# Performance work log

Hardware: AMD Instinct MI355X
Metric: run time of the kernel (lower is better)

The kernel has to match this reference:

```python
import jax, jax.numpy as jnp
import numpy as np

N, E, ND, ED, H, L = 50000, 800000, 6, 4, 128, 4


def _ln(x, g, b, eps=1e-5):
    m = x.mean(-1, keepdims=True)
    v = ((x - m) ** 2).mean(-1, keepdims=True)
    return (x - m) * jax.lax.rsqrt(v + eps) * g + b


def _block(x, w1, b1, g1, be1, w2, b2, g2, be2):
    # Linear -> LayerNorm -> GELU -> (Dropout=identity in eval) -> Linear -> LayerNorm -> GELU
    h = jax.nn.gelu(_ln(x @ w1 + b1, g1, be1), approximate=False)
    return jax.nn.gelu(_ln(h @ w2 + b2, g2, be2), approximate=False)


def setup_inputs() -> dict:
    key = jax.random.key(0)
    ks = iter(jax.random.split(key, 16))
    w = lambda *s: jax.random.normal(next(ks), s, jnp.float32) * 0.05
    z = lambda *s: jnp.zeros(s, jnp.float32)
    o = lambda *s: jnp.ones(s, jnp.float32)
    return {
        "x": jax.random.normal(next(ks), (N, ND), jnp.float32),
        "edge_index": jax.random.randint(next(ks), (2, E), 0, N),
        "edge_attr": jax.random.normal(next(ks), (E, ED), jnp.float32),
        "ne_w1": w(ND, H), "ne_b1": z(H), "ne_g1": o(H), "ne_be1": z(H),
        "ne_w2": w(H, H), "ne_b2": z(H), "ne_g2": o(H), "ne_be2": z(H),
        "ee_w1": w(ED, H), "ee_b1": z(H), "ee_g1": o(H), "ee_be1": z(H),
        "ee_w2": w(H, H), "ee_b2": z(H), "ee_g2": o(H), "ee_be2": z(H),
        "cv_w1": w(L, H, H), "cv_b1": z(L, H), "cv_g1": o(L, H), "cv_be1": z(L, H),
        "cv_w2": w(L, H, H), "cv_b2": z(L, H), "cv_g2": o(L, H), "cv_be2": z(L, H),
        "nm_g": o(L, H), "nm_b": z(L, H),
        "dh_w1": w(H, H // 2), "dh_b1": z(H // 2), "dh_g": o(H // 2), "dh_be": z(H // 2),
        "dh_w2": w(H // 2, 3), "dh_b2": z(3),
        "sh_w1": w(H, H // 2), "sh_b1": z(H // 2), "sh_g": o(H // 2), "sh_be": z(H // 2),
        "sh_w2": w(H // 2, 1), "sh_b2": z(1),
    }


def reference(x, edge_index, edge_attr,
              ne_w1, ne_b1, ne_g1, ne_be1, ne_w2, ne_b2, ne_g2, ne_be2,
              ee_w1, ee_b1, ee_g1, ee_be1, ee_w2, ee_b2, ee_g2, ee_be2,
              cv_w1, cv_b1, cv_g1, cv_be1, cv_w2, cv_b2, cv_g2, cv_be2,
              nm_g, nm_b,
              dh_w1, dh_b1, dh_g, dh_be, dh_w2, dh_b2,
              sh_w1, sh_b1, sh_g, sh_be, sh_w2, sh_b2):
    h = _block(x, ne_w1, ne_b1, ne_g1, ne_be1, ne_w2, ne_b2, ne_g2, ne_be2)           # [N, H]
    e = _block(edge_attr, ee_w1, ee_b1, ee_g1, ee_be1, ee_w2, ee_b2, ee_g2, ee_be2)   # [E, H]
    src, dst = edge_index[0], edge_index[1]
    for l in range(L):
        # GINEConv (eps=0): sum_j relu(x_j + e_ij), then MLP((1+eps)*x + aggr)
        msg = jax.nn.relu(h[src] + e)                         # [E, H] gather + edge add
        agg = jax.ops.segment_sum(msg, dst, num_segments=N)   # [N, H] scatter-add
        u = _block(h + agg, cv_w1[l], cv_b1[l], cv_g1[l], cv_be1[l],
                   cv_w2[l], cv_b2[l], cv_g2[l], cv_be2[l])
        h = h + jax.nn.gelu(_ln(u, nm_g[l], nm_b[l]), approximate=False)  # residual
    d = jax.nn.gelu(_ln(h @ dh_w1 + dh_b1, dh_g, dh_be), approximate=False)
    displacement = d @ dh_w2 + dh_b2                          # [N, 3]
    s = jax.nn.gelu(_ln(h @ sh_w1 + sh_b1, sh_g, sh_be), approximate=False)
    stress = jax.nn.softplus(s @ sh_w2 + sh_b2)               # [N, 1]
    return displacement, stress, h
```

## Files before the change

### kernel.cpp

```cpp
#include <hip/hip_runtime.h>
#include <hip/hip_bf16.h>

#define HD 128
#define TILE 64
#define ST 136

typedef __attribute__((ext_vector_type(8))) short bf16x8;
typedef __attribute__((ext_vector_type(4))) float f32x4;

__device__ __forceinline__ float gelu_f(float x) {
    float y = fabsf(x) * 0.70710678118654752f;
    float t = __builtin_amdgcn_rcpf(fmaf(0.3275911f, y, 1.0f));
    float p = t * fmaf(t, fmaf(t, fmaf(t, fmaf(t, 1.061405429f, -1.453152027f),
                                       1.421413741f), -0.284496736f), 0.254829592f);
    float E = fmaf(-p, __expf(-y * y), 1.0f);
    return 0.5f * x * (1.0f + copysignf(E, x));
}
__device__ __forceinline__ unsigned short f2bf(float f) {
    unsigned int x = __float_as_uint(f);
    x = x + 0x7fffu + ((x >> 16) & 1u);
    return (unsigned short)(x >> 16);
}
__device__ __forceinline__ unsigned int pk2bf(float lo, float hi) {
    return (unsigned int)f2bf(lo) | ((unsigned int)f2bf(hi) << 16);
}
__device__ __forceinline__ float bf2f(unsigned short u) {
    return __uint_as_float((unsigned int)u << 16);
}

__device__ __forceinline__ void mm_mfma(const unsigned short* sA, int wrow, int lane,
                                        const unsigned short* __restrict__ wt, f32x4 acc[8]) {
    int m = lane & 15, kb = lane >> 4;
    bf16x8 a[4];
#pragma unroll
    for (int kk = 0; kk < 4; ++kk)
        a[kk] = *(const bf16x8*)(sA + (wrow + m) * ST + kk * 32 + kb * 8);
#pragma unroll
    for (int n0 = 0; n0 < 8; ++n0) {
        f32x4 c = {0.f, 0.f, 0.f, 0.f};
#pragma unroll
        for (int kk = 0; kk < 4; ++kk) {
            bf16x8 b = *(const bf16x8*)(wt + ((size_t)((n0 * 4 + kk) * 64 + lane)) * 8);
            c = __builtin_amdgcn_mfma_f32_16x16x32_bf16(b, a[kk], c, 0, 0, 0);
        }
        acc[n0] = c;
    }
}

__device__ __forceinline__ void mm_mfma2(const unsigned short* sH, const unsigned short* sL,
                                         int wrow, int lane,
                                         const unsigned short* __restrict__ wt, f32x4 acc[8]) {
    int m = lane & 15, kb = lane >> 4;
    bf16x8 ah[4], al[4];
#pragma unroll
    for (int kk = 0; kk < 4; ++kk) {
        ah[kk] = *(const bf16x8*)(sH + (wrow + m) * ST + kk * 32 + kb * 8);
        al[kk] = *(const bf16x8*)(sL + (wrow + m) * ST + kk * 32 + kb * 8);
    }
#pragma unroll
    for (int n0 = 0; n0 < 8; ++n0) {
        f32x4 c = {0.f, 0.f, 0.f, 0.f};
#pragma unroll
        for (int kk = 0; kk < 4; ++kk) {
            bf16x8 b = *(const bf16x8*)(wt + ((size_t)((n0 * 4 + kk) * 64 + lane)) * 8);
            c = __builtin_amdgcn_mfma_f32_16x16x32_bf16(b, ah[kk], c, 0, 0, 0);
            c = __builtin_amdgcn_mfma_f32_16x16x32_bf16(b, al[kk], c, 0, 0, 0);
        }
        acc[n0] = c;
    }
}

__device__ __forceinline__ void bias_ln_gelu(f32x4 acc[8], float u[8][4],
                                             const float* bias, const float* g,
                                             const float* be, int kb) {
    float s = 0.f, ss = 0.f;
#pragma unroll
    for (int n0 = 0; n0 < 8; ++n0)
#pragma unroll
        for (int q = 0; q < 4; ++q) {
            float x = acc[n0][q] + bias[n0 * 16 + kb * 4 + q];
            u[n0][q] = x;
            s += x; ss += x * x;
        }
    s += __shfl_xor(s, 16); ss += __shfl_xor(ss, 16);
    s += __shfl_xor(s, 32); ss += __shfl_xor(ss, 32);
    float mean = s * (1.f / HD);
    float inv = rsqrtf(ss * (1.f / HD) - mean * mean + 1e-5f);
#pragma unroll
    for (int n0 = 0; n0 < 8; ++n0)
#pragma unroll
        for (int q = 0; q < 4; ++q) {
            int c = n0 * 16 + kb * 4 + q;
            u[n0][q] = gelu_f((u[n0][q] - mean) * inv * g[c] + be[c]);
        }
}

__global__ void prep_weights(const float* __restrict__ ne_w2, const float* __restrict__ ee_w2,
                             const float* __restrict__ cv_w1, const float* __restrict__ cv_w2,
                             unsigned short* __restrict__ wbf) {
    int mat = blockIdx.x;
    const float* src = (mat == 0) ? ne_w2
                     : (mat == 1) ? ee_w2
                     : (mat < 6)  ? cv_w1 + (size_t)(mat - 2) * HD * HD
                                  : cv_w2 + (size_t)(mat - 6) * HD * HD;
    unsigned short* dst = wbf + (size_t)mat * HD * HD;
    for (int i = threadIdx.x; i < HD * HD; i += 256) {
        int e = i & 7, lane = (i >> 3) & 63, f = i >> 9;
        int m = lane & 15, kb = lane >> 4;
        int n0 = f >> 2, kk = f & 3;
        int k = kk * 32 + kb * 8 + e;
        int c = n0 * 16 + m;
        dst[i] = f2bf(src[(size_t)k * HD + c]);
    }
}

template <int IN_DIM, bool EDGE>
__global__ __launch_bounds__(256) void encoder_mfma(
    const float* __restrict__ in, const float* __restrict__ w1,
    const float* __restrict__ b1, const float* __restrict__ g1,
    const float* __restrict__ be1, const unsigned short* __restrict__ wt2,
    const float* __restrict__ b2, const float* __restrict__ g2,
    const float* __restrict__ be2, float* __restrict__ h_out,
    unsigned short* __restrict__ e_perm, const int* __restrict__ pos, int rows) {
    __shared__ __align__(16) unsigned short s_A[TILE * ST];
    __shared__ float s_vec[6][HD];
    __shared__ int s_pos[TILE];

    int tid = threadIdx.x;
    int row0 = blockIdx.x * TILE;
    if (tid < HD) {
        s_vec[0][tid] = b1[tid]; s_vec[1][tid] = g1[tid]; s_vec[2][tid] = be1[tid];
        s_vec[3][tid] = b2[tid]; s_vec[4][tid] = g2[tid]; s_vec[5][tid] = be2[tid];
    }
    if (EDGE && tid < TILE) {
        int gr = row0 + tid;
        s_pos[tid] = (gr < rows) ? pos[gr] : 0;
    }
    __syncthreads();

    int tr = tid >> 4, tc = tid & 15;
    int r0 = tr * 4, c0 = tc * 8;
    float w1r[IN_DIM][8];
#pragma unroll
    for (int k = 0; k < IN_DIM; ++k) {
        float4 pa = *(const float4*)(w1 + (size_t)k * HD + c0);
        float4 pb = *(const float4*)(w1 + (size_t)k * HD + c0 + 4);
        w1r[k][0] = pa.x; w1r[k][1] = pa.y; w1r[k][2] = pa.z; w1r[k][3] = pa.w;
        w1r[k][4] = pb.x; w1r[k][5] = pb.y; w1r[k][6] = pb.z; w1r[k][7] = pb.w;
    }
    float v[4][8];
#pragma unroll
    for (int i = 0; i < 4; ++i)
#pragma unroll
        for (int j = 0; j < 8; ++j) v[i][j] = s_vec[0][c0 + j];
#pragma unroll
    for (int i = 0; i < 4; ++i) {
        int gr = min(row0 + r0 + i, rows - 1);
        float xr[IN_DIM];
        if constexpr (IN_DIM == 4) {
            float4 t4 = *(const float4*)(in + (size_t)gr * 4);
            xr[0] = t4.x; xr[1] = t4.y; xr[2] = t4.z; xr[3] = t4.w;
        } else {
#pragma unroll
            for (int k = 0; k < IN_DIM; ++k) xr[k] = in[(size_t)gr * IN_DIM + k];
        }
#pragma unroll
        for (int k = 0; k < IN_DIM; ++k)
#pragma unroll
            for (int j = 0; j < 8; ++j) v[i][j] = fmaf(xr[k], w1r[k][j], v[i][j]);
    }
#pragma unroll
    for (int i = 0; i < 4; ++i) {
        float s = 0.f, ss = 0.f;
#pragma unroll
        for (int j = 0; j < 8; ++j) { s += v[i][j]; ss += v[i][j] * v[i][j]; }
#pragma unroll
        for (int msk = 1; msk < 16; msk <<= 1) { s += __shfl_xor(s, msk); ss += __shfl_xor(ss, msk); }
        float mean = s * (1.f / HD);
        float inv = rsqrtf(ss * (1.f / HD) - mean * mean + 1e-5f);
#pragma unroll
        for (int j = 0; j < 8; ++j)
            v[i][j] = gelu_f((v[i][j] - mean) * inv * s_vec[1][c0 + j] + s_vec[2][c0 + j]);
        uint4 q4;
        q4.x = pk2bf(v[i][0], v[i][1]); q4.y = pk2bf(v[i][2], v[i][3]);
        q4.z = pk2bf(v[i][4], v[i][5]); q4.w = pk2bf(v[i][6], v[i][7]);
        *(uint4*)&s_A[(r0 + i) * ST + c0] = q4;
    }
    __syncthreads();

    int wave = tid >> 6, lane = tid & 63;
    int m = lane & 15, kb = lane >> 4;
    int wrow = wave * 16;
    f32x4 acc[8];
    mm_mfma(s_A, wrow, lane, wt2, acc);
    float u[8][4];
    bias_ln_gelu(acc, u, s_vec[3], s_vec[4], s_vec[5], kb);

    if (EDGE) {
        __syncthreads();
#pragma unroll
        for (int n0 = 0; n0 < 8; ++n0) {
            uint2 p;
            p.x = pk2bf(u[n0][0], u[n0][1]);
            p.y = pk2bf(u[n0][2], u[n0][3]);
            *(uint2*)&s_A[(wrow + m) * ST + n0 * 16 + kb * 4] = p;
        }
        __syncthreads();
#pragma unroll
        for (int i = 0; i < 4; ++i) {
            int c = tid + i * 256;
            int r = c >> 4, cc = (c & 15) * 8;
            int gr = row0 + r;
            if (gr < rows) {
                uint4 q4 = *(uint4*)&s_A[r * ST + cc];
                *(uint4*)(e_perm + (size_t)s_pos[r] * HD + cc) = q4;
            }
        }
    } else {
        int grow = row0 + wrow + m;
        if (grow < rows) {
#pragma unroll
            for (int n0 = 0; n0 < 8; ++n0)
                *(float4*)(h_out + (size_t)grow * HD + n0 * 16 + kb * 4) =
                    make_float4(u[n0][0], u[n0][1], u[n0][2], u[n0][3]);
        }
    }
}

__global__ __launch_bounds__(256) void conv_mfma(
    const unsigned short* __restrict__ tin_hi, const unsigned short* __restrict__ tin_lo,
    float* __restrict__ h,
    const unsigned short* __restrict__ wt1, const float* __restrict__ b1,
    const float* __restrict__ g1, const float* __restrict__ be1,
    const unsigned short* __restrict__ wt2, const float* __restrict__ b2,
    const float* __restrict__ g2, const float* __restrict__ be2,
    const float* __restrict__ nmg, const float* __restrict__ nmb, int rows) {
    __shared__ __align__(16) unsigned short s_A[TILE * ST];
    __shared__ __align__(16) unsigned short s_L[TILE * ST];
    __shared__ float s_vec[8][HD];

    int tid = threadIdx.x;
    int row0 = blockIdx.x * TILE;
    if (tid < HD) {
        s_vec[0][tid] = b1[tid];  s_vec[1][tid] = g1[tid];  s_vec[2][tid] = be1[tid];
        s_vec[3][tid] = b2[tid];  s_vec[4][tid] = g2[tid];  s_vec[5][tid] = be2[tid];
        s_vec[6][tid] = nmg[tid]; s_vec[7][tid] = nmb[tid];
    }
#pragma unroll
    for (int i = 0; i < 4; ++i) {
        int c = tid + i * 256;
        int r = c >> 4, cc = (c & 15) * 8;
        int gr = min(row0 + r, rows - 1);
        *(uint4*)&s_A[r * ST + cc] = *(const uint4*)(tin_hi + (size_t)gr * HD + cc);
        *(uint4*)&s_L[r * ST + cc] = *(const uint4*)(tin_lo + (size_t)gr * HD + cc);
    }
    __syncthreads();

    int wave = tid >> 6, lane = tid & 63;
    int m = lane & 15, kb = lane >> 4;
    int wrow = wave * 16;
    f32x4 acc[8];
    float u[8][4];

    mm_mfma2(s_A, s_L, wrow, lane, wt1, acc);
    bias_ln_gelu(acc, u, s_vec[0], s_vec[1], s_vec[2], kb);
    __syncthreads();
#pragma unroll
    for (int n0 = 0; n0 < 8; ++n0) {
        uint2 p;
        p.x = pk2bf(u[n0][0], u[n0][1]);
        p.y = pk2bf(u[n0][2], u[n0][3]);
        *(uint2*)&s_A[(wrow + m) * ST + n0 * 16 + kb * 4] = p;
    }
    __syncthreads();

    mm_mfma(s_A, wrow, lane, wt2, acc);
    bias_ln_gelu(acc, u, s_vec[3], s_vec[4], s_vec[5], kb);
    {
        float s = 0.f, ss = 0.f;
#pragma unroll
        for (int n0 = 0; n0 < 8; ++n0)
#pragma unroll
            for (int q = 0; q < 4; ++q) { s += u[n0][q]; ss += u[n0][q] * u[n0][q]; }
        s += __shfl_xor(s, 16); ss += __shfl_xor(ss, 16);
        s += __shfl_xor(s, 32); ss += __shfl_xor(ss, 32);
        float mean = s * (1.f / HD);
        float inv = rsqrtf(ss * (1.f / HD) - mean * mean + 1e-5f);
#pragma unroll
        for (int n0 = 0; n0 < 8; ++n0)
#pragma unroll
            for (int q = 0; q < 4; ++q) {
                int c = n0 * 16 + kb * 4 + q;
                u[n0][q] = gelu_f((u[n0][q] - mean) * inv * s_vec[6][c] + s_vec[7][c]);
            }
    }
    int grow = row0 + wrow + m;
    if (grow < rows) {
#pragma unroll
        for (int n0 = 0; n0 < 8; ++n0) {
            size_t idx = (size_t)grow * HD + n0 * 16 + kb * 4;
            float4 hv = *(const float4*)(h + idx);
            hv.x += u[n0][0]; hv.y += u[n0][1]; hv.z += u[n0][2]; hv.w += u[n0][3];
            *(float4*)(h + idx) = hv;
        }
    }
}

__global__ void zero_kernel(int* p, int n) {
    int i = blockIdx.x * 256 + threadIdx.x;
    if (i < n) p[i] = 0;
}
__global__ void hist_kernel(const int* __restrict__ dst, int* __restrict__ cnt, int n) {
    for (int i = blockIdx.x * 256 + threadIdx.x; i < n; i += gridDim.x * 256)
        atomicAdd(&cnt[dst[i]], 1);
}
__global__ __launch_bounds__(1024) void scan_block_kernel(
    const int* __restrict__ cnt, int* __restrict__ incl, int* __restrict__ bsum, int n) {
    __shared__ int buf[2][1024];
    int t = threadIdx.x;
    int i = blockIdx.x * 1024 + t;
    int v = (i < n) ? cnt[i] : 0;
    buf[0][t] = v;
    __syncthreads();
    int pin = 0;
    for (int off = 1; off < 1024; off <<= 1) {
        int x = buf[pin][t];
        if (t >= off) x += buf[pin][t - off];
        buf[pin ^ 1][t] = x;
        __syncthreads();
        pin ^= 1;
    }
    if (i < n) incl[i] = buf[pin][t];
    if (t == 1023) bsum[blockIdx.x] = buf[pin][t];
}
__global__ void scan_top_kernel(int* bsum, int nb) {
    int t = threadIdx.x;
    int v = (t < nb) ? bsum[t] : 0;
    int orig = v;
#pragma unroll
    for (int off = 1; off < 64; off <<= 1) {
        int y = __shfl_up(v, off);
        if (t >= off) v += y;
    }
    if (t < nb) bsum[t] = v - orig;
}
__global__ void add_off_kernel(int* __restrict__ offs, const int* __restrict__ bsum,
                               int* __restrict__ cursor, int n) {
    int i = blockIdx.x * 256 + threadIdx.x;
    if (i == 0) { offs[0] = 0; cursor[0] = 0; }
    if (i < n) {
        int v = offs[i + 1] + bsum[i >> 10];
        offs[i + 1] = v;
        if (i + 1 < n) cursor[i + 1] = v;
    }
}
__global__ void scatter_kernel(const int* __restrict__ srcArr, const int* __restrict__ dstArr,
                               int* __restrict__ cursor, int* __restrict__ pos,
                               int* __restrict__ esrc, int n) {
    for (int i = blockIdx.x * 256 + threadIdx.x; i < n; i += gridDim.x * 256) {
        int d = dstArr[i];
        int p = atomicAdd(&cursor[d], 1);
        pos[i] = p;
        esrc[p] = srcArr[i];
    }
}

__global__ __launch_bounds__(256) void aggregate_kernel(
    const float* __restrict__ h, const unsigned short* __restrict__ e,
    const int* __restrict__ offs, const int* __restrict__ esrc,
    unsigned short* __restrict__ tin_hi, unsigned short* __restrict__ tin_lo, int nnodes) {
    int wave = threadIdx.x >> 6, lane = threadIdx.x & 63;
    int n = blockIdx.x * 4 + wave;
    if (n >= nnodes) return;
    int beg = offs[n], end = offs[n + 1];
    float ax = 0.f, ay = 0.f;
    int i = beg;
    for (; i + 4 <= end; i += 4) {
        int s0 = esrc[i], s1 = esrc[i + 1], s2 = esrc[i + 2], s3 = esrc[i + 3];
        float2 h0 = *(const float2*)(h + (size_t)s0 * HD + 2 * lane);
        float2 h1 = *(const float2*)(h + (size_t)s1 * HD + 2 * lane);
        float2 h2 = *(const float2*)(h + (size_t)s2 * HD + 2 * lane);
        float2 h3 = *(const float2*)(h + (size_t)s3 * HD + 2 * lane);
        unsigned int e0 = *(const unsigned int*)(e + (size_t)(i + 0) * HD + 2 * lane);
        unsigned int e1 = *(const unsigned int*)(e + (size_t)(i + 1) * HD + 2 * lane);
        unsigned int e2 = *(const unsigned int*)(e + (size_t)(i + 2) * HD + 2 * lane);
        unsigned int e3 = *(const unsigned int*)(e + (size_t)(i + 3) * HD + 2 * lane);
        ax += fmaxf(h0.x + __uint_as_float(e0 << 16), 0.f);
        ay += fmaxf(h0.y + __uint_as_float(e0 & 0xffff0000u), 0.f);
        ax += fmaxf(h1.x + __uint_as_float(e1 << 16), 0.f);
        ay += fmaxf(h1.y + __uint_as_float(e1 & 0xffff0000u), 0.f);
        ax += fmaxf(h2.x + __uint_as_float(e2 << 16), 0.f);
        ay += fmaxf(h2.y + __uint_as_float(e2 & 0xffff0000u), 0.f);
        ax += fmaxf(h3.x + __uint_as_float(e3 << 16), 0.f);
        ay += fmaxf(h3.y + __uint_as_float(e3 & 0xffff0000u), 0.f);
    }
    for (; i < end; ++i) {
        int src = esrc[i];
        float2 hv = *(const float2*)(h + (size_t)src * HD + 2 * lane);
        unsigned int ue = *(const unsigned int*)(e + (size_t)i * HD + 2 * lane);
        ax += fmaxf(hv.x + __uint_as_float(ue << 16), 0.f);
        ay += fmaxf(hv.y + __uint_as_float(ue & 0xffff0000u), 0.f);
    }
    float2 hn = *(const float2*)(h + (size_t)n * HD + 2 * lane);
    float tx = hn.x + ax, ty = hn.y + ay;
    unsigned short hx = f2bf(tx), hy = f2bf(ty);
    float lx = tx - bf2f(hx), ly = ty - bf2f(hy);
    *(unsigned int*)(tin_hi + (size_t)n * HD + 2 * lane) =
        (unsigned int)hx | ((unsigned int)hy << 16);
    *(unsigned int*)(tin_lo + (size_t)n * HD + 2 * lane) = pk2bf(lx, ly);
}

__global__ __launch_bounds__(256) void head_kernel(
    const float* __restrict__ h, const float* __restrict__ dw1,
    const float* __restrict__ db1, const float* __restrict__ dg,
    const float* __restrict__ dbe, const float* __restrict__ dw2,
    const float* __restrict__ db2, const float* __restrict__ sw1,
    const float* __restrict__ sb1, const float* __restrict__ sg,
    const float* __restrict__ sbe, const float* __restrict__ sw2,
    const float* __restrict__ sb2, float* __restrict__ out, int nnodes) {
    __shared__ float s_wd[HD * 64];
    __shared__ float s_ws[HD * 64];
    __shared__ float s_vd[3][64];
    __shared__ float s_vs[3][64];
    __shared__ float s_w2d[64 * 3];
    __shared__ float s_w2s[64];
    __shared__ float s_h[4][HD];
    __shared__ float s_b2[4];

    int tid = threadIdx.x;
    for (int i = tid; i < HD * 64; i += 256) { s_wd[i] = dw1[i]; s_ws[i] = sw1[i]; }
    if (tid < 64) {
        s_vd[0][tid] = db1[tid]; s_vd[1][tid] = dg[tid]; s_vd[2][tid] = dbe[tid];
        s_vs[0][tid] = sb1[tid]; s_vs[1][tid] = sg[tid]; s_vs[2][tid] = sbe[tid];
        s_w2s[tid] = sw2[tid];
    }
    if (tid < 64 * 3) s_w2d[tid] = dw2[tid];
    if (tid == 0) { s_b2[0] = db2[0]; s_b2[1] = db2[1]; s_b2[2] = db2[2]; s_b2[3] = sb2[0]; }
    __syncthreads();

    int wave = tid >> 6, lane = tid & 63;
    float* disp = out;
    float* stress = out + (size_t)nnodes * 3;
    float* hout = out + (size_t)nnodes * 4;

    for (int n = blockIdx.x * 4 + wave; n < nnodes; n += gridDim.x * 4) {
        float2 hv = *(const float2*)(h + (size_t)n * HD + lane * 2);
        *(float2*)(hout + (size_t)n * HD + lane * 2) = hv;
        s_h[wave][lane * 2] = hv.x;
        s_h[wave][lane * 2 + 1] = hv.y;
        float accd = s_vd[0][lane], accs = s_vs[0][lane];
        for (int k = 0; k < HD; ++k) {
            float hx = s_h[wave][k];
            accd = fmaf(hx, s_wd[k * 64 + lane], accd);
            accs = fmaf(hx, s_ws[k * 64 + lane], accs);
        }
        float s = accd, ss = accd * accd;
#pragma unroll
        for (int msk = 1; msk < 64; msk <<= 1) { s += __shfl_xor(s, msk); ss += __shfl_xor(ss, msk); }
        float mean = s * (1.f / 64), inv = rsqrtf(ss * (1.f / 64) - mean * mean + 1e-5f);
        float d = gelu_f((accd - mean) * inv * s_vd[1][lane] + s_vd[2][lane]);
        s = accs; ss = accs * accs;
#pragma unroll
        for (int msk = 1; msk < 64; msk <<= 1) { s += __shfl_xor(s, msk); ss += __shfl_xor(ss, msk); }
        mean = s * (1.f / 64); inv = rsqrtf(ss * (1.f / 64) - mean * mean + 1e-5f);
        float sv = gelu_f((accs - mean) * inv * s_vs[1][lane] + s_vs[2][lane]);
        float p0 = d * s_w2d[lane * 3 + 0];
        float p1 = d * s_w2d[lane * 3 + 1];
        float p2 = d * s_w2d[lane * 3 + 2];
        float ps = sv * s_w2s[lane];
#pragma unroll
        for (int msk = 1; msk < 64; msk <<= 1) {
            p0 += __shfl_xor(p0, msk); p1 += __shfl_xor(p1, msk);
            p2 += __shfl_xor(p2, msk); ps += __shfl_xor(ps, msk);
        }
        if (lane == 0) {
            disp[(size_t)n * 3 + 0] = p0 + s_b2[0];
            disp[(size_t)n * 3 + 1] = p1 + s_b2[1];
            disp[(size_t)n * 3 + 2] = p2 + s_b2[2];
            float xs = ps + s_b2[3];
            stress[n] = fmaxf(xs, 0.f) + log1pf(expf(-fabsf(xs)));
        }
    }
}

extern "C" void kernel_launch(void* const* d_in, const int* in_sizes, int n_in,
                              void* d_out, int out_size, void* d_ws, size_t ws_size,
                              hipStream_t stream) {
    const float* x = (const float*)d_in[0];
    const int* ei = (const int*)d_in[1];
    const float* ea = (const float*)d_in[2];
    const float* ne_w1 = (const float*)d_in[3];
    const float* ne_b1 = (const float*)d_in[4];
    const float* ne_g1 = (const float*)d_in[5];
    const float* ne_be1 = (const float*)d_in[6];
    const float* ne_w2 = (const float*)d_in[7];
    const float* ne_b2 = (const float*)d_in[8];
    const float* ne_g2 = (const float*)d_in[9];
    const float* ne_be2 = (const float*)d_in[10];
    const float* ee_w1 = (const float*)d_in[11];
    const float* ee_b1 = (const float*)d_in[12];
    const float* ee_g1 = (const float*)d_in[13];
    const float* ee_be1 = (const float*)d_in[14];
    const float* ee_w2 = (const float*)d_in[15];
    const float* ee_b2 = (const float*)d_in[16];
    const float* ee_g2 = (const float*)d_in[17];
    const float* ee_be2 = (const float*)d_in[18];
    const float* cv_w1 = (const float*)d_in[19];
    const float* cv_b1 = (const float*)d_in[20];
    const float* cv_g1 = (const float*)d_in[21];
    const float* cv_be1 = (const float*)d_in[22];
    const float* cv_w2 = (const float*)d_in[23];
    const float* cv_b2 = (const float*)d_in[24];
    const float* cv_g2 = (const float*)d_in[25];
    const float* cv_be2 = (const float*)d_in[26];
    const float* nm_g = (const float*)d_in[27];
    const float* nm_b = (const float*)d_in[28];
    const float* dh_w1 = (const float*)d_in[29];
    const float* dh_b1 = (const float*)d_in[30];
    const float* dh_g = (const float*)d_in[31];
    const float* dh_be = (const float*)d_in[32];
    const float* dh_w2 = (const float*)d_in[33];
    const float* dh_b2 = (const float*)d_in[34];
    const float* sh_w1 = (const float*)d_in[35];
    const float* sh_b1 = (const float*)d_in[36];
    const float* sh_g = (const float*)d_in[37];
    const float* sh_be = (const float*)d_in[38];
    const float* sh_w2 = (const float*)d_in[39];
    const float* sh_b2 = (const float*)d_in[40];

    int N = in_sizes[0] / 6;
    int E = in_sizes[1] / 2;

    char* wp = (char*)d_ws;
    auto take = [&](size_t bytes) {
        char* p = wp;
        wp += (bytes + 255) & ~(size_t)255;
        return p;
    };
    unsigned short* e_perm = (unsigned short*)take((size_t)E * HD * 2);
    float* h = (float*)take((size_t)N * HD * 4);
    unsigned short* tin_hi = (unsigned short*)take((size_t)N * HD * 2);
    unsigned short* tin_lo = (unsigned short*)take((size_t)N * HD * 2);
    unsigned short* wbf = (unsigned short*)take((size_t)10 * HD * HD * 2);
    int* cnt = (int*)take((size_t)N * 4);
    int* offs = (int*)take((size_t)(N + 1) * 4);
    int* cursor = (int*)take((size_t)N * 4);
    int* bsum = (int*)take(256);
    int* pos = (int*)take((size_t)E * 4);
    int* esrc = (int*)take((size_t)E * 4);

    const int* srcArr = ei;
    const int* dstArr = ei + E;

    int nbN = (N + TILE - 1) / TILE;
    int nbE = (E + TILE - 1) / TILE;

    prep_weights<<<10, 256, 0, stream>>>(ne_w2, ee_w2, cv_w1, cv_w2, wbf);
    zero_kernel<<<(N + 255) / 256, 256, 0, stream>>>(cnt, N);
    hist_kernel<<<2048, 256, 0, stream>>>(dstArr, cnt, E);
    int nsb = (N + 1023) / 1024;
    scan_block_kernel<<<nsb, 1024, 0, stream>>>(cnt, offs + 1, bsum, N);
    scan_top_kernel<<<1, 64, 0, stream>>>(bsum, nsb);
    add_off_kernel<<<(N + 255) / 256, 256, 0, stream>>>(offs, bsum, cursor, N);
    scatter_kernel<<<2048, 256, 0, stream>>>(srcArr, dstArr, cursor, pos, esrc, E);

    encoder_mfma<6, false><<<nbN, 256, 0, stream>>>(
        x, ne_w1, ne_b1, ne_g1, ne_be1, wbf + 0 * HD * HD, ne_b2, ne_g2, ne_be2,
        h, nullptr, nullptr, N);
    encoder_mfma<4, true><<<nbE, 256, 0, stream>>>(
        ea, ee_w1, ee_b1, ee_g1, ee_be1, wbf + 1 * HD * HD, ee_b2, ee_g2, ee_be2,
        nullptr, e_perm, pos, E);

    for (int l = 0; l < 4; ++l) {
        aggregate_kernel<<<(N + 3) / 4, 256, 0, stream>>>(h, e_perm, offs, esrc,
                                                          tin_hi, tin_lo, N);
        conv_mfma<<<nbN, 256, 0, stream>>>(
            tin_hi, tin_lo, h, wbf + (size_t)(2 + l) * HD * HD, cv_b1 + l * HD,
            cv_g1 + l * HD, cv_be1 + l * HD, wbf + (size_t)(6 + l) * HD * HD,
            cv_b2 + l * HD, cv_g2 + l * HD, cv_be2 + l * HD,
            nm_g + l * HD, nm_b + l * HD, N);
    }

    head_kernel<<<1024, 256, 0, stream>>>(h, dh_w1, dh_b1, dh_g, dh_be, dh_w2, dh_b2,
                                          sh_w1, sh_b1, sh_g, sh_be, sh_w2, sh_b2,
                                          (float*)d_out, N);
}
```

Measured before the change: 879.4 us.

## Fuse neighbor aggregation into conv MFMA kernel with ping-pong h buffers

```diff
diff --git a/kernel.cpp b/kernel.cpp
--- a/kernel.cpp
+++ b/kernel.cpp
@@ -227,9 +227,10 @@
     }
 }
 
-__global__ __launch_bounds__(256) void conv_mfma(
-    const unsigned short* __restrict__ tin_hi, const unsigned short* __restrict__ tin_lo,
-    float* __restrict__ h,
+__global__ __launch_bounds__(256) void agg_conv_mfma(
+    const float* __restrict__ h_old, float* __restrict__ h_new,
+    const unsigned short* __restrict__ e,
+    const int* __restrict__ offs, const int* __restrict__ esrc,
     const unsigned short* __restrict__ wt1, const float* __restrict__ b1,
     const float* __restrict__ g1, const float* __restrict__ be1,
     const unsigned short* __restrict__ wt2, const float* __restrict__ b2,
@@ -246,17 +247,55 @@
         s_vec[3][tid] = b2[tid];  s_vec[4][tid] = g2[tid];  s_vec[5][tid] = be2[tid];
         s_vec[6][tid] = nmg[tid]; s_vec[7][tid] = nmb[tid];
     }
-#pragma unroll
-    for (int i = 0; i < 4; ++i) {
-        int c = tid + i * 256;
-        int r = c >> 4, cc = (c & 15) * 8;
-        int gr = min(row0 + r, rows - 1);
-        *(uint4*)&s_A[r * ST + cc] = *(const uint4*)(tin_hi + (size_t)gr * HD + cc);
-        *(uint4*)&s_L[r * ST + cc] = *(const uint4*)(tin_lo + (size_t)gr * HD + cc);
-    }
-    __syncthreads();
-
     int wave = tid >> 6, lane = tid & 63;
+
+    for (int t = 0; t < 16; ++t) {
+        int row = wave * 16 + t;
+        int n = row0 + row;
+        if (n < rows) {
+            int beg = offs[n], end = offs[n + 1];
+            float ax = 0.f, ay = 0.f;
+            int i = beg;
+            for (; i + 4 <= end; i += 4) {
+                int s0 = esrc[i], s1 = esrc[i + 1], s2 = esrc[i + 2], s3 = esrc[i + 3];
+                float2 h0 = *(const float2*)(h_old + (size_t)s0 * HD + 2 * lane);
+                float2 h1 = *(const float2*)(h_old + (size_t)s1 * HD + 2 * lane);
+                float2 h2 = *(const float2*)(h_old + (size_t)s2 * HD + 2 * lane);
+                float2 h3 = *(const float2*)(h_old + (size_t)s3 * HD + 2 * lane);
+                unsigned int e0 = *(const unsigned int*)(e + (size_t)(i + 0) * HD + 2 * lane);
+                unsigned int e1 = *(const unsigned int*)(e + (size_t)(i + 1) * HD + 2 * lane);
+                unsigned int e2 = *(const unsigned int*)(e + (size_t)(i + 2) * HD + 2 * lane);
+                unsigned int e3 = *(const unsigned int*)(e + (size_t)(i + 3) * HD + 2 * lane);
+                ax += fmaxf(h0.x + __uint_as_float(e0 << 16), 0.f);
+                ay += fmaxf(h0.y + __uint_as_float(e0 & 0xffff0000u), 0.f);
+                ax += fmaxf(h1.x + __uint_as_float(e1 << 16), 0.f);
+                ay += fmaxf(h1.y + __uint_as_float(e1 & 0xffff0000u), 0.f);
+                ax += fmaxf(h2.x + __uint_as_float(e2 << 16), 0.f);
+                ay += fmaxf(h2.y + __uint_as_float(e2 & 0xffff0000u), 0.f);
+                ax += fmaxf(h3.x + __uint_as_float(e3 << 16), 0.f);
+                ay += fmaxf(h3.y + __uint_as_float(e3 & 0xffff0000u), 0.f);
+            }
+            for (; i < end; ++i) {
+                int src = esrc[i];
+                float2 hv = *(const float2*)(h_old + (size_t)src * HD + 2 * lane);
+                unsigned int ue = *(const unsigned int*)(e + (size_t)i * HD + 2 * lane);
+                ax += fmaxf(hv.x + __uint_as_float(ue << 16), 0.f);
+                ay += fmaxf(hv.y + __uint_as_float(ue & 0xffff0000u), 0.f);
+            }
+            float2 hn = *(const float2*)(h_old + (size_t)n * HD + 2 * lane);
+            float tx = hn.x + ax, ty = hn.y + ay;
+            unsigned short hx = f2bf(tx), hy = f2bf(ty);
+            *(unsigned int*)&s_A[row * ST + 2 * lane] =
+                (unsigned int)hx | ((unsigned int)hy << 16);
+            *(unsigned int*)&s_L[row * ST + 2 * lane] =
+                pk2bf(tx - bf2f(hx), ty - bf2f(hy));
+        } else {
+            *(unsigned int*)&s_A[row * ST + 2 * lane] = 0;
+            *(unsigned int*)&s_L[row * ST + 2 * lane] = 0;
+        }
+    }
+    __syncthreads();
+
     int m = lane & 15, kb = lane >> 4;
     int wrow = wave * 16;
     f32x4 acc[8];
@@ -299,9 +338,9 @@
 #pragma unroll
         for (int n0 = 0; n0 < 8; ++n0) {
             size_t idx = (size_t)grow * HD + n0 * 16 + kb * 4;
-            float4 hv = *(const float4*)(h + idx);
+            float4 hv = *(const float4*)(h_old + idx);
             hv.x += u[n0][0]; hv.y += u[n0][1]; hv.z += u[n0][2]; hv.w += u[n0][3];
-            *(float4*)(h + idx) = hv;
+            *(float4*)(h_new + idx) = hv;
         }
     }
 }
@@ -363,51 +402,6 @@
         pos[i] = p;
         esrc[p] = srcArr[i];
     }
-}
-
-__global__ __launch_bounds__(256) void aggregate_kernel(
-    const float* __restrict__ h, const unsigned short* __restrict__ e,
-    const int* __restrict__ offs, const int* __restrict__ esrc,
-    unsigned short* __restrict__ tin_hi, unsigned short* __restrict__ tin_lo, int nnodes) {
-    int wave = threadIdx.x >> 6, lane = threadIdx.x & 63;
-    int n = blockIdx.x * 4 + wave;
-    if (n >= nnodes) return;
-    int beg = offs[n], end = offs[n + 1];
-    float ax = 0.f, ay = 0.f;
-    int i = beg;
-    for (; i + 4 <= end; i += 4) {
-        int s0 = esrc[i], s1 = esrc[i + 1], s2 = esrc[i + 2], s3 = esrc[i + 3];
-        float2 h0 = *(const float2*)(h + (size_t)s0 * HD + 2 * lane);
-        float2 h1 = *(const float2*)(h + (size_t)s1 * HD + 2 * lane);
-        float2 h2 = *(const float2*)(h + (size_t)s2 * HD + 2 * lane);
-        float2 h3 = *(const float2*)(h + (size_t)s3 * HD + 2 * lane);
-        unsigned int e0 = *(const unsigned int*)(e + (size_t)(i + 0) * HD + 2 * lane);
-        unsigned int e1 = *(const unsigned int*)(e + (size_t)(i + 1) * HD + 2 * lane);
-        unsigned int e2 = *(const unsigned int*)(e + (size_t)(i + 2) * HD + 2 * lane);
-        unsigned int e3 = *(const unsigned int*)(e + (size_t)(i + 3) * HD + 2 * lane);
-        ax += fmaxf(h0.x + __uint_as_float(e0 << 16), 0.f);
-        ay += fmaxf(h0.y + __uint_as_float(e0 & 0xffff0000u), 0.f);
-        ax += fmaxf(h1.x + __uint_as_float(e1 << 16), 0.f);
-        ay += fmaxf(h1.y + __uint_as_float(e1 & 0xffff0000u), 0.f);
-        ax += fmaxf(h2.x + __uint_as_float(e2 << 16), 0.f);
-        ay += fmaxf(h2.y + __uint_as_float(e2 & 0xffff0000u), 0.f);
-        ax += fmaxf(h3.x + __uint_as_float(e3 << 16), 0.f);
-        ay += fmaxf(h3.y + __uint_as_float(e3 & 0xffff0000u), 0.f);
-    }
-    for (; i < end; ++i) {
-        int src = esrc[i];
-        float2 hv = *(const float2*)(h + (size_t)src * HD + 2 * lane);
-        unsigned int ue = *(const unsigned int*)(e + (size_t)i * HD + 2 * lane);
-        ax += fmaxf(hv.x + __uint_as_float(ue << 16), 0.f);
-        ay += fmaxf(hv.y + __uint_as_float(ue & 0xffff0000u), 0.f);
-    }
-    float2 hn = *(const float2*)(h + (size_t)n * HD + 2 * lane);
-    float tx = hn.x + ax, ty = hn.y + ay;
-    unsigned short hx = f2bf(tx), hy = f2bf(ty);
-    float lx = tx - bf2f(hx), ly = ty - bf2f(hy);
-    *(unsigned int*)(tin_hi + (size_t)n * HD + 2 * lane) =
-        (unsigned int)hx | ((unsigned int)hy << 16);
-    *(unsigned int*)(tin_lo + (size_t)n * HD + 2 * lane) = pk2bf(lx, ly);
 }
 
 __global__ __launch_bounds__(256) void head_kernel(
@@ -538,9 +532,8 @@
         return p;
     };
     unsigned short* e_perm = (unsigned short*)take((size_t)E * HD * 2);
-    float* h = (float*)take((size_t)N * HD * 4);
-    unsigned short* tin_hi = (unsigned short*)take((size_t)N * HD * 2);
-    unsigned short* tin_lo = (unsigned short*)take((size_t)N * HD * 2);
+    float* h0 = (float*)take((size_t)N * HD * 4);
+    float* h1 = (float*)take((size_t)N * HD * 4);
     unsigned short* wbf = (unsigned short*)take((size_t)10 * HD * HD * 2);
     int* cnt = (int*)take((size_t)N * 4);
     int* offs = (int*)take((size_t)(N + 1) * 4);
@@ -566,22 +559,23 @@
 
     encoder_mfma<6, false><<<nbN, 256, 0, stream>>>(
         x, ne_w1, ne_b1, ne_g1, ne_be1, wbf + 0 * HD * HD, ne_b2, ne_g2, ne_be2,
-        h, nullptr, nullptr, N);
+        h0, nullptr, nullptr, N);
     encoder_mfma<4, true><<<nbE, 256, 0, stream>>>(
         ea, ee_w1, ee_b1, ee_g1, ee_be1, wbf + 1 * HD * HD, ee_b2, ee_g2, ee_be2,
         nullptr, e_perm, pos, E);
 
+    float* hbuf[2] = {h0, h1};
     for (int l = 0; l < 4; ++l) {
-        aggregate_kernel<<<(N + 3) / 4, 256, 0, stream>>>(h, e_perm, offs, esrc,
-                                                          tin_hi, tin_lo, N);
-        conv_mfma<<<nbN, 256, 0, stream>>>(
-            tin_hi, tin_lo, h, wbf + (size_t)(2 + l) * HD * HD, cv_b1 + l * HD,
-            cv_g1 + l * HD, cv_be1 + l * HD, wbf + (size_t)(6 + l) * HD * HD,
-            cv_b2 + l * HD, cv_g2 + l * HD, cv_be2 + l * HD,
-            nm_g + l * HD, nm_b + l * HD, N);
-    }
-
-    head_kernel<<<1024, 256, 0, stream>>>(h, dh_w1, dh_b1, dh_g, dh_be, dh_w2, dh_b2,
+        float* h_old = hbuf[l & 1];
+        float* h_new = hbuf[(l + 1) & 1];
+        agg_conv_mfma<<<nbN, 256, 0, stream>>>(
+            h_old, h_new, e_perm, offs, esrc, wbf + (size_t)(2 + l) * HD * HD,
+            cv_b1 + l * HD, cv_g1 + l * HD, cv_be1 + l * HD,
+            wbf + (size_t)(6 + l) * HD * HD, cv_b2 + l * HD, cv_g2 + l * HD,
+            cv_be2 + l * HD, nm_g + l * HD, nm_b + l * HD, N);
+    }
+
+    head_kernel<<<1024, 256, 0, stream>>>(h0, dh_w1, dh_b1, dh_g, dh_be, dh_w2, dh_b2,
                                           sh_w1, sh_b1, sh_g, sh_be, sh_w2, sh_b2,
                                           (float*)d_out, N);
 }
```

Result: slower. 1.079 ms (+22.6%).
